# Performance work log

Hardware: AMD Instinct MI355X
Metric: run time of the kernel (lower is better)

Reference implementation:

```python
import jax, jax.numpy as jnp
import numpy as np

MARGIN = 2.0
N_STREAM = 4
BRANCH_WEIGHT = np.ones(N_STREAM, dtype=np.float32)  # default branch_weight = [1.0]*n_stream
ALPHA = 1.0 / N_STREAM  # MultistreamLoss default alpha
BETA = 1.0              # MultistreamLoss default beta
EPS = 1e-4


def _ranking(preds, labels):
    # sum over pairs i<j of relu(-(p[j]-p[i]) * sign(l[j]-l[i]) + margin)
    n = preds.shape[0]
    d = preds[None, :] - preds[:, None]          # d[i, j] = p[j] - p[i]
    s = jnp.sign(labels[None, :] - labels[:, None])
    h = jax.nn.relu(-d * s + MARGIN)             # [n, n]
    mask = jnp.triu(jnp.ones((n, n), dtype=bool), k=1)  # j > i
    return jnp.sum(jnp.where(mask, h, jnp.zeros((), h.dtype)))


def setup_inputs() -> dict:
    key = jax.random.key(0)
    k1, k2, k3 = jax.random.split(key, 3)
    n = 4096
    scores = jax.random.normal(k1, (N_STREAM, n), dtype=jnp.float32)
    pred = jax.random.normal(k2, (n,), dtype=jnp.float32)
    label = jax.random.normal(k3, (n,), dtype=jnp.float32)
    return {"scores": scores, "pred": pred, "label": label}


def reference(scores, pred, label):
    # branch ranking losses, one per stream
    branch = jax.vmap(lambda s: _ranking(s, label))(scores)       # [N_STREAM]
    branch_loss = jnp.sum(jnp.asarray(BRANCH_WEIGHT) * branch)

    # BatchRankingMSE_Loss (alpha=None -> 1.0, beta=None -> grad-norm ratio, no renorm)
    mse = jnp.mean((pred - label) ** 2)
    rank = _ranking(pred, label)
    g1 = jnp.linalg.norm(jax.grad(lambda p: jnp.mean((p - label) ** 2))(pred))
    g2 = jnp.linalg.norm(jax.grad(lambda p: _ranking(p, label))(pred))
    beta_w = jax.lax.stop_gradient(g1 / (g2 + EPS))  # computed under no_grad in torch
    pred_loss = 1.0 * mse + beta_w * rank

    return ALPHA * branch_loss + BETA * pred_loss
```

## Files before the change

### kernel.cpp

```cpp
#include <hip/hip_runtime.h>
#include <math.h>

#define N 4096
#define MARGINF 2.0f
#define EPSF 1e-4f

typedef _Float16 f16x2 __attribute__((ext_vector_type(2)));

__device__ __forceinline__ unsigned f2u(f16x2 h){ return __builtin_bit_cast(unsigned, h); }
__device__ __forceinline__ f16x2 u2f(unsigned u){ return __builtin_bit_cast(f16x2, u); }
__device__ __forceinline__ unsigned pku(float a, float b){
    return __builtin_bit_cast(unsigned, __builtin_amdgcn_cvt_pkrtz(a, b));
}
__device__ __forceinline__ f16x2 pk2(float a){ return u2f(pku(a, a)); }
__device__ __forceinline__ float fdot2(f16x2 a, f16x2 b, float c){
    return __builtin_amdgcn_fdot2(a, b, c, false);
}
__device__ __forceinline__ f16x2 c_one(){ return u2f(0x3C003C00u); }
__device__ __forceinline__ f16x2 c_two(){ return u2f(0x40004000u); }
__device__ __forceinline__ f16x2 c_zero(){ return u2f(0u); }
__device__ __forceinline__ f16x2 c_big(){ return u2f(0x7BFF7BFFu); }

constexpr int CC = 128;
constexpr int NCHUNK = N / CC;
constexpr int RTS = 1024;
constexpr int RTP = 512;
constexpr int SCORE_PER_STREAM = 80;
constexpr int NSCORE_BLK = 4 * SCORE_PER_STREAM;
constexpr int NPRED_BLK = (N / RTP) * NCHUNK;
constexpr int NBLK = NSCORE_BLK + NPRED_BLK;
constexpr int PRED_PART = 512;
constexpr int G16_BYTE_OFF = 4096;


__device__ __forceinline__ void body2(unsigned lm2u, unsigned pm2u,
                                      f16x2 lk2, f16x2 rk2, float& acc){
    const f16x2 ld2 = u2f(lm2u) - lk2;
    const unsigned sgn = f2u(ld2) & 0x80008000u;
    const f16x2 pd2 = u2f(pm2u) - rk2;
    const f16x2 x2 = u2f(f2u(pd2) ^ sgn);
    const f16x2 m2 = __builtin_elementwise_max(c_two() - x2, c_zero());
    acc = fdot2(m2, c_one(), acc);
}

__device__ __forceinline__ void body2m(unsigned lm2u, unsigned pm2u,
                                       f16x2 lk2, f16x2 rk2, int d, float& acc){
    const f16x2 ld2 = u2f(lm2u) - lk2;
    const unsigned sgn = f2u(ld2) & 0x80008000u;
    const f16x2 pd2 = u2f(pm2u) - rk2;
    const f16x2 x2 = u2f(f2u(pd2) ^ sgn);
    const f16x2 m2 = __builtin_elementwise_max(c_two() - x2, c_zero());
    const unsigned mu = (d >= 0) ? ((d > 0) ? 0x3C003C00u : 0x3C000000u) : 0u;
    acc = fdot2(m2, u2f(mu), acc);
}

__device__ __forceinline__ void body2g(unsigned lm2u, unsigned pm2u,
                                       f16x2 lk2, f16x2 rk2, float& acc, float& gacc){
    const f16x2 ld2 = u2f(lm2u) - lk2;
    const unsigned sgn = f2u(ld2) & 0x80008000u;
    const f16x2 pd2 = u2f(pm2u) - rk2;
    const f16x2 x2 = u2f(f2u(pd2) ^ sgn);
    const f16x2 m2 = __builtin_elementwise_max(c_two() - x2, c_zero());
    acc = fdot2(m2, c_one(), acc);
    const f16x2 ind2 = __builtin_elementwise_min(m2 * c_big(), c_one());
    gacc = fdot2(u2f(f2u(ind2) ^ sgn), c_one(), gacc);
}

__global__ __launch_bounds__(256) void pair_kernel(
    const float* __restrict__ scores, const float* __restrict__ pred,
    const float* __restrict__ label, float* __restrict__ ws)
{
    __shared__ unsigned lab16[CC / 2];
    __shared__ unsigned col16[CC / 2];
    __shared__ float red[4];

    const int bid = blockIdx.x;
    const int tid = threadIdx.x;
    const bool isScore = (bid < NSCORE_BLK);

    int ti, c, rb;
    const float* __restrict__ colsrc;
    if (isScore) {
        const int stream = bid / SCORE_PER_STREAM;
        const int b = bid % SCORE_PER_STREAM;
        if      (b < 32) { ti = 0; c = b; }
        else if (b < 56) { ti = 1; c = 8  + (b - 32); }
        else if (b < 72) { ti = 2; c = 16 + (b - 56); }
        else             { ti = 3; c = 24 + (b - 72); }
        rb = ti * RTS;
        colsrc = scores + stream * N;
    } else {
        const int q = bid - NSCORE_BLK;
        ti = q >> 5;
        c  = q & 31;
        rb = ti * RTP;
        colsrc = pred;
    }
    const int c0 = c * CC;

    if (tid < CC / 2) {
        const float2 lf = *(const float2*)&label[c0 + 2 * tid];
        lab16[tid] = pku(lf.x, lf.y);
    } else if (tid < CC) {
        const int q = tid - CC / 2;
        const float2 pf = *(const float2*)&colsrc[c0 + 2 * q];
        col16[q] = pku(pf.x, pf.y);
    }
    __syncthreads();

    float blocksum;

    if (isScore) {
        int r[4]; f16x2 rk2[4], lk2[4];
        #pragma unroll
        for (int k = 0; k < 4; ++k) {
            r[k] = rb + tid + 256 * k;
            rk2[k] = pk2(colsrc[r[k]]);
            lk2[k] = pk2(label[r[k]]);
        }
        float acc[8] = {0.f,0.f,0.f,0.f,0.f,0.f,0.f,0.f};

        if (c >= 8 * (ti + 1)) {
            #pragma unroll 4
            for (int q = 0; q < CC / 16; ++q) {
                const uint4 l4a = *(const uint4*)&lab16[q * 8];
                const uint4 s4a = *(const uint4*)&col16[q * 8];
                const uint4 l4b = *(const uint4*)&lab16[q * 8 + 4];
                const uint4 s4b = *(const uint4*)&col16[q * 8 + 4];
                #pragma unroll
                for (int k = 0; k < 4; ++k) {
                    body2(l4a.x, s4a.x, lk2[k], rk2[k], acc[k]);
                    body2(l4a.y, s4a.y, lk2[k], rk2[k], acc[4 + k]);
                    body2(l4a.z, s4a.z, lk2[k], rk2[k], acc[k]);
                    body2(l4a.w, s4a.w, lk2[k], rk2[k], acc[4 + k]);
                    body2(l4b.x, s4b.x, lk2[k], rk2[k], acc[k]);
                    body2(l4b.y, s4b.y, lk2[k], rk2[k], acc[4 + k]);
                    body2(l4b.z, s4b.z, lk2[k], rk2[k], acc[k]);
                    body2(l4b.w, s4b.w, lk2[k], rk2[k], acc[4 + k]);
                }
            }
        } else {
            #pragma unroll 4
            for (int q = 0; q < CC / 8; ++q) {
                const uint4 l4 = *(const uint4*)&lab16[q * 4];
                const uint4 s4 = *(const uint4*)&col16[q * 4];
                const int cb = c0 + q * 8;
                #pragma unroll
                for (int k = 0; k < 4; ++k) {
                    body2m(l4.x, s4.x, lk2[k], rk2[k], cb + 0 - r[k], acc[k]);
                    body2m(l4.y, s4.y, lk2[k], rk2[k], cb + 2 - r[k], acc[4 + k]);
                    body2m(l4.z, s4.z, lk2[k], rk2[k], cb + 4 - r[k], acc[k]);
                    body2m(l4.w, s4.w, lk2[k], rk2[k], cb + 6 - r[k], acc[4 + k]);
                }
            }
        }
        blocksum = (acc[0] + acc[1]) + (acc[2] + acc[3])
                 + (acc[4] + acc[5]) + (acc[6] + acc[7]);
    } else {
        int r[2]; f16x2 rk2[2], lk2[2];
        #pragma unroll
        for (int k = 0; k < 2; ++k) {
            r[k] = rb + tid + 256 * k;
            rk2[k] = pk2(pred[r[k]]);
            lk2[k] = pk2(label[r[k]]);
        }
        float acc[4] = {0.f,0.f,0.f,0.f};
        float grd[4] = {0.f,0.f,0.f,0.f};

        #pragma unroll 4
        for (int q = 0; q < CC / 8; ++q) {
            const uint4 l4 = *(const uint4*)&lab16[q * 4];
            const uint4 s4 = *(const uint4*)&col16[q * 4];
            #pragma unroll
            for (int k = 0; k < 2; ++k) {
                body2g(l4.x, s4.x, lk2[k], rk2[k], acc[k],     grd[k]);
                body2g(l4.y, s4.y, lk2[k], rk2[k], acc[2 + k], grd[2 + k]);
                body2g(l4.z, s4.z, lk2[k], rk2[k], acc[k],     grd[k]);
                body2g(l4.w, s4.w, lk2[k], rk2[k], acc[2 + k], grd[2 + k]);
            }
        }
        unsigned short* g16 = (unsigned short*)((char*)ws + G16_BYTE_OFF);
        #pragma unroll
        for (int k = 0; k < 2; ++k) {
            float g = grd[k] + grd[2 + k];
            if ((r[k] >> 7) == c) g -= 1.0f;
            const _Float16 gh = (_Float16)g;
            g16[r[k] * NCHUNK + c] = __builtin_bit_cast(unsigned short, gh);
        }
        blocksum = (acc[0] + acc[1]) + (acc[2] + acc[3]);
    }

    #pragma unroll
    for (int off = 32; off > 0; off >>= 1)
        blocksum += __shfl_xor(blocksum, off, 64);
    const int wid = tid >> 6;
    const int lane = tid & 63;
    if (lane == 0) red[wid] = blocksum;
    __syncthreads();
    if (tid == 0) {
        const float total = red[0] + red[1] + red[2] + red[3];
        if (isScore) ws[bid] = total;
        else         ws[PRED_PART + (bid - NSCORE_BLK)] = total;
    }
}

__global__ __launch_bounds__(256) void finalize_kernel(
    const float* __restrict__ pred, const float* __restrict__ label,
    const float* __restrict__ ws, float* __restrict__ out)
{
    __shared__ float lds[16];
    const int tid = threadIdx.x;
    const unsigned short* g16 = (const unsigned short*)((const char*)ws + G16_BYTE_OFF);

    float sse = 0.f, g2sq = 0.f;
    #pragma unroll
    for (int k = 0; k < 16; ++k) {
        const int i = k * 256 + tid;
        const float d = pred[i] - label[i];
        sse += d * d;
        const uint4* gp = (const uint4*)(g16 + i * NCHUNK);
        const uint4 a = gp[0], b = gp[1], cq = gp[2], e = gp[3];
        const f16x2 s0 = (u2f(a.x) + u2f(a.y)) + (u2f(a.z) + u2f(a.w));
        const f16x2 s1 = (u2f(b.x) + u2f(b.y)) + (u2f(b.z) + u2f(b.w));
        const f16x2 s2 = (u2f(cq.x) + u2f(cq.y)) + (u2f(cq.z) + u2f(cq.w));
        const f16x2 s3 = (u2f(e.x) + u2f(e.y)) + (u2f(e.z) + u2f(e.w));
        const f16x2 t0 = s0 + s1, t1 = s2 + s3;
        const float g = ((float)t0.x + (float)t0.y) + ((float)t1.x + (float)t1.y);
        g2sq += g * g;
    }

    float br = ws[tid] + ((tid < 64) ? ws[256 + tid] : 0.f);
    float pr = ws[PRED_PART + tid];

    #pragma unroll
    for (int off = 32; off > 0; off >>= 1) {
        sse  += __shfl_xor(sse,  off, 64);
        g2sq += __shfl_xor(g2sq, off, 64);
        br   += __shfl_xor(br,   off, 64);
        pr   += __shfl_xor(pr,   off, 64);
    }
    const int wid = tid >> 6;
    const int lane = tid & 63;
    if (lane == 0) {
        lds[wid] = sse; lds[4 + wid] = g2sq;
        lds[8 + wid] = br; lds[12 + wid] = pr;
    }
    __syncthreads();
    if (tid == 0) {
        const float sseT  = lds[0] + lds[1] + lds[2] + lds[3];
        const float g2sqT = lds[4] + lds[5] + lds[6] + lds[7];
        const float brT   = lds[8] + lds[9] + lds[10] + lds[11];
        const float prT   = lds[12] + lds[13] + lds[14] + lds[15];
        const float rankp = (prT - (float)N * MARGINF) * 0.5f;
        const float mse = sseT / (float)N;
        const float g1 = (2.0f / (float)N) * sqrtf(sseT);
        const float g2 = sqrtf(g2sqT);
        const float beta = g1 / (g2 + EPSF);
        out[0] = 0.25f * brT + mse + beta * rankp;
    }
}

extern "C" void kernel_launch(void* const* d_in, const int* in_sizes, int n_in,
                              void* d_out, int out_size, void* d_ws, size_t ws_size,
                              hipStream_t stream) {
    const float* scores = (const float*)d_in[0];
    const float* pred   = (const float*)d_in[1];
    const float* label  = (const float*)d_in[2];
    float* ws  = (float*)d_ws;
    float* out = (float*)d_out;

    pair_kernel<<<NBLK, 256, 0, stream>>>(scores, pred, label, ws);
    finalize_kernel<<<1, 256, 0, stream>>>(pred, label, ws, out);
}
```

Baseline: 24.73 us.

## Fuse pair and finalize kernels using per-block done tags and a spinning last block

```diff
diff --git a/kernel.cpp b/kernel.cpp
--- a/kernel.cpp
+++ b/kernel.cpp
@@ -30,7 +30,9 @@
 constexpr int NPRED_BLK = (N / RTP) * NCHUNK;
 constexpr int NBLK = NSCORE_BLK + NPRED_BLK;
 constexpr int PRED_PART = 512;
-constexpr int G16_BYTE_OFF = 4096;
+constexpr unsigned DONE_TAG = 0x3FA0B7C4u;
+constexpr int TAG_BYTE_OFF = 8192;
+constexpr int G16_BYTE_OFF = 16384;
 
 
 __device__ __forceinline__ void body2(unsigned lm2u, unsigned pm2u,
@@ -66,18 +68,11 @@
     gacc = fdot2(u2f(f2u(ind2) ^ sgn), c_one(), gacc);
 }
 
-__global__ __launch_bounds__(256) void pair_kernel(
+__device__ __forceinline__ float pair_phase(
     const float* __restrict__ scores, const float* __restrict__ pred,
-    const float* __restrict__ label, float* __restrict__ ws)
+    const float* __restrict__ label, float* __restrict__ ws,
+    unsigned* lab16, unsigned* col16, int bid, int tid, bool isScore)
 {
-    __shared__ unsigned lab16[CC / 2];
-    __shared__ unsigned col16[CC / 2];
-    __shared__ float red[4];
-
-    const int bid = blockIdx.x;
-    const int tid = threadIdx.x;
-    const bool isScore = (bid < NSCORE_BLK);
-
     int ti, c, rb;
     const float* __restrict__ colsrc;
     if (isScore) {
@@ -189,36 +184,22 @@
         }
         blocksum = (acc[0] + acc[1]) + (acc[2] + acc[3]);
     }
-
-    #pragma unroll
-    for (int off = 32; off > 0; off >>= 1)
-        blocksum += __shfl_xor(blocksum, off, 64);
-    const int wid = tid >> 6;
-    const int lane = tid & 63;
-    if (lane == 0) red[wid] = blocksum;
-    __syncthreads();
-    if (tid == 0) {
-        const float total = red[0] + red[1] + red[2] + red[3];
-        if (isScore) ws[bid] = total;
-        else         ws[PRED_PART + (bid - NSCORE_BLK)] = total;
-    }
-}
-
-__global__ __launch_bounds__(256) void finalize_kernel(
+    return blocksum;
+}
+
+__device__ __forceinline__ void finalize_phase(
     const float* __restrict__ pred, const float* __restrict__ label,
-    const float* __restrict__ ws, float* __restrict__ out)
+    const float* __restrict__ ws, float* __restrict__ out,
+    float* red, int tid)
 {
-    __shared__ float lds[16];
-    const int tid = threadIdx.x;
-    const unsigned short* g16 = (const unsigned short*)((const char*)ws + G16_BYTE_OFF);
-
+    const unsigned short* g16r = (const unsigned short*)((const char*)ws + G16_BYTE_OFF);
     float sse = 0.f, g2sq = 0.f;
     #pragma unroll
     for (int k = 0; k < 16; ++k) {
         const int i = k * 256 + tid;
         const float d = pred[i] - label[i];
         sse += d * d;
-        const uint4* gp = (const uint4*)(g16 + i * NCHUNK);
+        const uint4* gp = (const uint4*)(g16r + i * NCHUNK);
         const uint4 a = gp[0], b = gp[1], cq = gp[2], e = gp[3];
         const f16x2 s0 = (u2f(a.x) + u2f(a.y)) + (u2f(a.z) + u2f(a.w));
         const f16x2 s1 = (u2f(b.x) + u2f(b.y)) + (u2f(b.z) + u2f(b.w));
@@ -242,15 +223,15 @@
     const int wid = tid >> 6;
     const int lane = tid & 63;
     if (lane == 0) {
-        lds[wid] = sse; lds[4 + wid] = g2sq;
-        lds[8 + wid] = br; lds[12 + wid] = pr;
+        red[wid] = sse; red[4 + wid] = g2sq;
+        red[8 + wid] = br; red[12 + wid] = pr;
     }
     __syncthreads();
     if (tid == 0) {
-        const float sseT  = lds[0] + lds[1] + lds[2] + lds[3];
-        const float g2sqT = lds[4] + lds[5] + lds[6] + lds[7];
-        const float brT   = lds[8] + lds[9] + lds[10] + lds[11];
-        const float prT   = lds[12] + lds[13] + lds[14] + lds[15];
+        const float sseT  = red[0] + red[1] + red[2] + red[3];
+        const float g2sqT = red[4] + red[5] + red[6] + red[7];
+        const float brT   = red[8] + red[9] + red[10] + red[11];
+        const float prT   = red[12] + red[13] + red[14] + red[15];
         const float rankp = (prT - (float)N * MARGINF) * 0.5f;
         const float mse = sseT / (float)N;
         const float g1 = (2.0f / (float)N) * sqrtf(sseT);
@@ -258,6 +239,58 @@
         const float beta = g1 / (g2 + EPSF);
         out[0] = 0.25f * brT + mse + beta * rankp;
     }
+}
+
+__global__ __launch_bounds__(256) void fused_kernel(
+    const float* __restrict__ scores, const float* __restrict__ pred,
+    const float* __restrict__ label, float* __restrict__ ws,
+    float* __restrict__ out)
+{
+    __shared__ unsigned lab16[CC / 2];
+    __shared__ unsigned col16[CC / 2];
+    __shared__ float red[16];
+
+    const int bid = blockIdx.x;
+    const int tid = threadIdx.x;
+    unsigned* tags = (unsigned*)((char*)ws + TAG_BYTE_OFF);
+
+    if (bid < NBLK) {
+        const bool isScore = (bid < NSCORE_BLK);
+        float blocksum = pair_phase(scores, pred, label, ws, lab16, col16,
+                                    bid, tid, isScore);
+        #pragma unroll
+        for (int off = 32; off > 0; off >>= 1)
+            blocksum += __shfl_xor(blocksum, off, 64);
+        const int wid = tid >> 6;
+        const int lane = tid & 63;
+        if (lane == 0) red[wid] = blocksum;
+        __syncthreads();
+        if (tid == 0) {
+            const float total = red[0] + red[1] + red[2] + red[3];
+            if (isScore) ws[bid] = total;
+            else         ws[PRED_PART + (bid - NSCORE_BLK)] = total;
+        }
+        __threadfence();
+        __syncthreads();
+        if (tid == 0)
+            __hip_atomic_store(&tags[bid], DONE_TAG, __ATOMIC_RELEASE,
+                               __HIP_MEMORY_SCOPE_AGENT);
+        return;
+    }
+
+    for (int i = tid; i < NBLK; i += 256) {
+        while (__hip_atomic_load(&tags[i], __ATOMIC_ACQUIRE,
+                                 __HIP_MEMORY_SCOPE_AGENT) != DONE_TAG) {
+            __builtin_amdgcn_s_sleep(2);
+        }
+    }
+    __syncthreads();
+    __threadfence();
+    finalize_phase(pred, label, ws, out, red, tid);
+    __syncthreads();
+    for (int i = tid; i < NBLK; i += 256)
+        __hip_atomic_store(&tags[i], 0u, __ATOMIC_RELAXED,
+                           __HIP_MEMORY_SCOPE_AGENT);
 }
 
 extern "C" void kernel_launch(void* const* d_in, const int* in_sizes, int n_in,
@@ -269,6 +302,5 @@
     float* ws  = (float*)d_ws;
     float* out = (float*)d_out;
 
-    pair_kernel<<<NBLK, 256, 0, stream>>>(scores, pred, label, ws);
-    finalize_kernel<<<1, 256, 0, stream>>>(pred, label, ws, out);
-}
+    fused_kernel<<<NBLK + 1, 256, 0, stream>>>(scores, pred, label, ws, out);
+}
```

New measurement: 76.09 us. +207.7%, slower.

## Fuse pair and finalize kernels using an atomic counter and in-kernel finalizer block

Applied to the files above, without the earlier changes.

```diff
diff --git a/kernel.cpp b/kernel.cpp
--- a/kernel.cpp
+++ b/kernel.cpp
@@ -4,6 +4,7 @@
 #define N 4096
 #define MARGINF 2.0f
 #define EPSF 1e-4f
+#define SCOPE_AGENT __HIP_MEMORY_SCOPE_AGENT
 
 typedef _Float16 f16x2 __attribute__((ext_vector_type(2)));
 
@@ -22,16 +23,16 @@
 __device__ __forceinline__ f16x2 c_big(){ return u2f(0x7BFF7BFFu); }
 
 constexpr int CC = 128;
-constexpr int NCHUNK = N / CC;
+constexpr int SCORE_PER_STREAM = 80;
+constexpr int NPRED_BLK = 128;
+constexpr int NSCORE_BLK = 4 * SCORE_PER_STREAM;
+constexpr int NPROD = NPRED_BLK + NSCORE_BLK;
 constexpr int RTS = 1024;
-constexpr int RTP = 512;
-constexpr int SCORE_PER_STREAM = 80;
-constexpr int NSCORE_BLK = 4 * SCORE_PER_STREAM;
-constexpr int NPRED_BLK = (N / RTP) * NCHUNK;
-constexpr int NBLK = NSCORE_BLK + NPRED_BLK;
-constexpr int PRED_PART = 512;
-constexpr int G16_BYTE_OFF = 4096;
-
+
+constexpr int CTR_OFF = 0;
+constexpr int A_OFF   = 64;
+constexpr int B_OFF   = 640;
+constexpr int C_OFF   = 832;
 
 __device__ __forceinline__ void body2(unsigned lm2u, unsigned pm2u,
                                       f16x2 lk2, f16x2 rk2, float& acc){
@@ -66,77 +67,167 @@
     gacc = fdot2(u2f(f2u(ind2) ^ sgn), c_one(), gacc);
 }
 
-__global__ __launch_bounds__(256) void pair_kernel(
+__global__ __launch_bounds__(256) void fused_kernel(
     const float* __restrict__ scores, const float* __restrict__ pred,
-    const float* __restrict__ label, float* __restrict__ ws)
+    const float* __restrict__ label, float* __restrict__ ws,
+    float* __restrict__ out)
 {
-    __shared__ unsigned lab16[CC / 2];
-    __shared__ unsigned col16[CC / 2];
-    __shared__ float red[4];
-
+    __shared__ unsigned shm[2 * 2080];
+    __shared__ float red[16];
+
+    unsigned* wsu = (unsigned*)ws;
     const int bid = blockIdx.x;
     const int tid = threadIdx.x;
-    const bool isScore = (bid < NSCORE_BLK);
-
-    int ti, c, rb;
-    const float* __restrict__ colsrc;
-    if (isScore) {
-        const int stream = bid / SCORE_PER_STREAM;
-        const int b = bid % SCORE_PER_STREAM;
-        if      (b < 32) { ti = 0; c = b; }
-        else if (b < 56) { ti = 1; c = 8  + (b - 32); }
-        else if (b < 72) { ti = 2; c = 16 + (b - 56); }
-        else             { ti = 3; c = 24 + (b - 72); }
-        rb = ti * RTS;
-        colsrc = scores + stream * N;
+
+    if (bid == 0) {
+        if (tid == 0) {
+            const unsigned snap = __hip_atomic_load(wsu + CTR_OFF, __ATOMIC_RELAXED,
+                                                    SCOPE_AGENT);
+            unsigned guard = 0;
+            while ((__hip_atomic_load(wsu + CTR_OFF, __ATOMIC_RELAXED, SCOPE_AGENT)
+                    - snap) < (unsigned)NPROD) {
+                __builtin_amdgcn_s_sleep(8);
+                if (++guard > (1u << 27)) break;
+            }
+            __threadfence();
+        }
+        __syncthreads();
+
+        float br = 0.f, pr = 0.f, g2sq = 0.f, sse = 0.f;
+        {
+            const int b1 = 1 + tid;
+            const float a1 = __uint_as_float(__hip_atomic_load(
+                wsu + A_OFF + b1, __ATOMIC_RELAXED, SCOPE_AGENT));
+            if (b1 <= NPRED_BLK) pr += a1; else br += a1;
+            const int b2 = 257 + tid;
+            if (b2 <= NPROD) {
+                br += __uint_as_float(__hip_atomic_load(
+                    wsu + A_OFF + b2, __ATOMIC_RELAXED, SCOPE_AGENT));
+            }
+            if (tid < NPRED_BLK) {
+                g2sq = __uint_as_float(__hip_atomic_load(
+                    wsu + B_OFF + 1 + tid, __ATOMIC_RELAXED, SCOPE_AGENT));
+                sse  = __uint_as_float(__hip_atomic_load(
+                    wsu + C_OFF + 1 + tid, __ATOMIC_RELAXED, SCOPE_AGENT));
+            }
+        }
+        #pragma unroll
+        for (int off = 32; off > 0; off >>= 1) {
+            br   += __shfl_xor(br,   off, 64);
+            pr   += __shfl_xor(pr,   off, 64);
+            g2sq += __shfl_xor(g2sq, off, 64);
+            sse  += __shfl_xor(sse,  off, 64);
+        }
+        const int wid = tid >> 6;
+        const int lane = tid & 63;
+        if (lane == 0) {
+            red[wid] = br; red[4 + wid] = pr;
+            red[8 + wid] = g2sq; red[12 + wid] = sse;
+        }
+        __syncthreads();
+        if (tid == 0) {
+            const float brT   = red[0] + red[1] + red[2] + red[3];
+            const float prT   = red[4] + red[5] + red[6] + red[7];
+            const float g2sqT = red[8] + red[9] + red[10] + red[11];
+            const float sseT  = red[12] + red[13] + red[14] + red[15];
+            const float rankp = (prT - (float)N * MARGINF) * 0.5f;
+            const float mse = sseT / (float)N;
+            const float g1 = (2.0f / (float)N) * sqrtf(sseT);
+            const float g2 = sqrtf(g2sqT);
+            const float beta = g1 / (g2 + EPSF);
+            out[0] = 0.25f * brT + mse + beta * rankp;
+        }
+        return;
+    }
+
+    const bool isPred = (bid <= NPRED_BLK);
+    float rank_total, g2sq_total = 0.f, sse_total = 0.f;
+
+    if (isPred) {
+        const int rb = (bid - 1) * 32;
+        #pragma unroll
+        for (int q = 0; q < 8; ++q) {
+            const int j = q * 256 + tid;
+            const float2 lf = *(const float2*)&label[2 * j];
+            shm[q * 260 + tid] = pku(lf.x, lf.y);
+            const float2 pf = *(const float2*)&pred[2 * j];
+            shm[2080 + q * 260 + tid] = pku(pf.x, pf.y);
+        }
+        __syncthreads();
+
+        const int rowofs = tid >> 3;
+        const int cg = tid & 7;
+        const int r = rb + rowofs;
+        const f16x2 rk2 = pk2(pred[r]);
+        const f16x2 lk2 = pk2(label[r]);
+        const unsigned base = cg * 260;
+
+        float acc0 = 0.f, acc1 = 0.f, g0 = 0.f, g1v = 0.f;
+        #pragma unroll 4
+        for (int it = 0; it < 64; ++it) {
+            const uint4 l4 = *(const uint4*)&shm[base + it * 4];
+            const uint4 s4 = *(const uint4*)&shm[2080 + base + it * 4];
+            body2g(l4.x, s4.x, lk2, rk2, acc0, g0);
+            body2g(l4.y, s4.y, lk2, rk2, acc1, g1v);
+            body2g(l4.z, s4.z, lk2, rk2, acc0, g0);
+            body2g(l4.w, s4.w, lk2, rk2, acc1, g1v);
+        }
+        rank_total = acc0 + acc1;
+        float g = g0 + g1v;
+        if (cg == (r >> 9)) g -= 1.0f;
+        g += __shfl_xor(g, 1, 64);
+        g += __shfl_xor(g, 2, 64);
+        g += __shfl_xor(g, 4, 64);
+        if (cg == 0) {
+            g2sq_total = g * g;
+            const float d = pred[r] - label[r];
+            sse_total = d * d;
+        }
     } else {
-        const int q = bid - NSCORE_BLK;
-        ti = q >> 5;
-        c  = q & 31;
-        rb = ti * RTP;
-        colsrc = pred;
-    }
-    const int c0 = c * CC;
-
-    if (tid < CC / 2) {
-        const float2 lf = *(const float2*)&label[c0 + 2 * tid];
-        lab16[tid] = pku(lf.x, lf.y);
-    } else if (tid < CC) {
-        const int q = tid - CC / 2;
-        const float2 pf = *(const float2*)&colsrc[c0 + 2 * q];
-        col16[q] = pku(pf.x, pf.y);
-    }
-    __syncthreads();
-
-    float blocksum;
-
-    if (isScore) {
+        const int b = bid - 1 - NPRED_BLK;
+        const int stream = b / SCORE_PER_STREAM;
+        const int t = b % SCORE_PER_STREAM;
+        int ti, c;
+        if      (t < 32) { ti = 0; c = t; }
+        else if (t < 56) { ti = 1; c = 8  + (t - 32); }
+        else if (t < 72) { ti = 2; c = 16 + (t - 56); }
+        else             { ti = 3; c = 24 + (t - 72); }
+        const float* __restrict__ p = scores + stream * N;
+        const int c0 = c * CC;
+        unsigned* lab16 = shm;
+        unsigned* col16 = shm + 2080;
+
+        if (tid < CC / 2) {
+            const float2 lf = *(const float2*)&label[c0 + 2 * tid];
+            lab16[tid] = pku(lf.x, lf.y);
+        } else if (tid < CC) {
+            const int q = tid - CC / 2;
+            const float2 pf = *(const float2*)&p[c0 + 2 * q];
+            col16[q] = pku(pf.x, pf.y);
+        }
+        __syncthreads();
+
+        const int rb = ti * RTS;
         int r[4]; f16x2 rk2[4], lk2[4];
         #pragma unroll
         for (int k = 0; k < 4; ++k) {
             r[k] = rb + tid + 256 * k;
-            rk2[k] = pk2(colsrc[r[k]]);
+            rk2[k] = pk2(p[r[k]]);
             lk2[k] = pk2(label[r[k]]);
         }
         float acc[8] = {0.f,0.f,0.f,0.f,0.f,0.f,0.f,0.f};
 
         if (c >= 8 * (ti + 1)) {
             #pragma unroll 4
-            for (int q = 0; q < CC / 16; ++q) {
-                const uint4 l4a = *(const uint4*)&lab16[q * 8];
-                const uint4 s4a = *(const uint4*)&col16[q * 8];
-                const uint4 l4b = *(const uint4*)&lab16[q * 8 + 4];
-                const uint4 s4b = *(const uint4*)&col16[q * 8 + 4];
+            for (int q = 0; q < CC / 8; ++q) {
+                const uint4 l4 = *(const uint4*)&lab16[q * 4];
+                const uint4 s4 = *(const uint4*)&col16[q * 4];
                 #pragma unroll
                 for (int k = 0; k < 4; ++k) {
-                    body2(l4a.x, s4a.x, lk2[k], rk2[k], acc[k]);
-                    body2(l4a.y, s4a.y, lk2[k], rk2[k], acc[4 + k]);
-                    body2(l4a.z, s4a.z, lk2[k], rk2[k], acc[k]);
-                    body2(l4a.w, s4a.w, lk2[k], rk2[k], acc[4 + k]);
-                    body2(l4b.x, s4b.x, lk2[k], rk2[k], acc[k]);
-                    body2(l4b.y, s4b.y, lk2[k], rk2[k], acc[4 + k]);
-                    body2(l4b.z, s4b.z, lk2[k], rk2[k], acc[k]);
-                    body2(l4b.w, s4b.w, lk2[k], rk2[k], acc[4 + k]);
+                    body2(l4.x, s4.x, lk2[k], rk2[k], acc[k]);
+                    body2(l4.y, s4.y, lk2[k], rk2[k], acc[4 + k]);
+                    body2(l4.z, s4.z, lk2[k], rk2[k], acc[k]);
+                    body2(l4.w, s4.w, lk2[k], rk2[k], acc[4 + k]);
                 }
             }
         } else {
@@ -154,109 +245,35 @@
                 }
             }
         }
-        blocksum = (acc[0] + acc[1]) + (acc[2] + acc[3])
-                 + (acc[4] + acc[5]) + (acc[6] + acc[7]);
-    } else {
-        int r[2]; f16x2 rk2[2], lk2[2];
-        #pragma unroll
-        for (int k = 0; k < 2; ++k) {
-            r[k] = rb + tid + 256 * k;
-            rk2[k] = pk2(pred[r[k]]);
-            lk2[k] = pk2(label[r[k]]);
-        }
-        float acc[4] = {0.f,0.f,0.f,0.f};
-        float grd[4] = {0.f,0.f,0.f,0.f};
-
-        #pragma unroll 4
-        for (int q = 0; q < CC / 8; ++q) {
-            const uint4 l4 = *(const uint4*)&lab16[q * 4];
-            const uint4 s4 = *(const uint4*)&col16[q * 4];
-            #pragma unroll
-            for (int k = 0; k < 2; ++k) {
-                body2g(l4.x, s4.x, lk2[k], rk2[k], acc[k],     grd[k]);
-                body2g(l4.y, s4.y, lk2[k], rk2[k], acc[2 + k], grd[2 + k]);
-                body2g(l4.z, s4.z, lk2[k], rk2[k], acc[k],     grd[k]);
-                body2g(l4.w, s4.w, lk2[k], rk2[k], acc[2 + k], grd[2 + k]);
-            }
-        }
-        unsigned short* g16 = (unsigned short*)((char*)ws + G16_BYTE_OFF);
-        #pragma unroll
-        for (int k = 0; k < 2; ++k) {
-            float g = grd[k] + grd[2 + k];
-            if ((r[k] >> 7) == c) g -= 1.0f;
-            const _Float16 gh = (_Float16)g;
-            g16[r[k] * NCHUNK + c] = __builtin_bit_cast(unsigned short, gh);
-        }
-        blocksum = (acc[0] + acc[1]) + (acc[2] + acc[3]);
-    }
-
-    #pragma unroll
-    for (int off = 32; off > 0; off >>= 1)
-        blocksum += __shfl_xor(blocksum, off, 64);
-    const int wid = tid >> 6;
-    const int lane = tid & 63;
-    if (lane == 0) red[wid] = blocksum;
-    __syncthreads();
-    if (tid == 0) {
-        const float total = red[0] + red[1] + red[2] + red[3];
-        if (isScore) ws[bid] = total;
-        else         ws[PRED_PART + (bid - NSCORE_BLK)] = total;
-    }
-}
-
-__global__ __launch_bounds__(256) void finalize_kernel(
-    const float* __restrict__ pred, const float* __restrict__ label,
-    const float* __restrict__ ws, float* __restrict__ out)
-{
-    __shared__ float lds[16];
-    const int tid = threadIdx.x;
-    const unsigned short* g16 = (const unsigned short*)((const char*)ws + G16_BYTE_OFF);
-
-    float sse = 0.f, g2sq = 0.f;
-    #pragma unroll
-    for (int k = 0; k < 16; ++k) {
-        const int i = k * 256 + tid;
-        const float d = pred[i] - label[i];
-        sse += d * d;
-        const uint4* gp = (const uint4*)(g16 + i * NCHUNK);
-        const uint4 a = gp[0], b = gp[1], cq = gp[2], e = gp[3];
-        const f16x2 s0 = (u2f(a.x) + u2f(a.y)) + (u2f(a.z) + u2f(a.w));
-        const f16x2 s1 = (u2f(b.x) + u2f(b.y)) + (u2f(b.z) + u2f(b.w));
-        const f16x2 s2 = (u2f(cq.x) + u2f(cq.y)) + (u2f(cq.z) + u2f(cq.w));
-        const f16x2 s3 = (u2f(e.x) + u2f(e.y)) + (u2f(e.z) + u2f(e.w));
-        const f16x2 t0 = s0 + s1, t1 = s2 + s3;
-        const float g = ((float)t0.x + (float)t0.y) + ((float)t1.x + (float)t1.y);
-        g2sq += g * g;
-    }
-
-    float br = ws[tid] + ((tid < 64) ? ws[256 + tid] : 0.f);
-    float pr = ws[PRED_PART + tid];
+        rank_total = (acc[0] + acc[1]) + (acc[2] + acc[3])
+                   + (acc[4] + acc[5]) + (acc[6] + acc[7]);
+    }
 
     #pragma unroll
     for (int off = 32; off > 0; off >>= 1) {
-        sse  += __shfl_xor(sse,  off, 64);
-        g2sq += __shfl_xor(g2sq, off, 64);
-        br   += __shfl_xor(br,   off, 64);
-        pr   += __shfl_xor(pr,   off, 64);
+        rank_total += __shfl_xor(rank_total, off, 64);
+        g2sq_total += __shfl_xor(g2sq_total, off, 64);
+        sse_total  += __shfl_xor(sse_total,  off, 64);
     }
     const int wid = tid >> 6;
     const int lane = tid & 63;
     if (lane == 0) {
-        lds[wid] = sse; lds[4 + wid] = g2sq;
-        lds[8 + wid] = br; lds[12 + wid] = pr;
+        red[wid] = rank_total; red[4 + wid] = g2sq_total; red[8 + wid] = sse_total;
     }
     __syncthreads();
     if (tid == 0) {
-        const float sseT  = lds[0] + lds[1] + lds[2] + lds[3];
-        const float g2sqT = lds[4] + lds[5] + lds[6] + lds[7];
-        const float brT   = lds[8] + lds[9] + lds[10] + lds[11];
-        const float prT   = lds[12] + lds[13] + lds[14] + lds[15];
-        const float rankp = (prT - (float)N * MARGINF) * 0.5f;
-        const float mse = sseT / (float)N;
-        const float g1 = (2.0f / (float)N) * sqrtf(sseT);
-        const float g2 = sqrtf(g2sqT);
-        const float beta = g1 / (g2 + EPSF);
-        out[0] = 0.25f * brT + mse + beta * rankp;
+        const float rankT = red[0] + red[1] + red[2] + red[3];
+        __hip_atomic_store(wsu + A_OFF + bid, __float_as_uint(rankT),
+                           __ATOMIC_RELAXED, SCOPE_AGENT);
+        if (isPred) {
+            const float g2T  = red[4] + red[5] + red[6] + red[7];
+            const float sseT = red[8] + red[9] + red[10] + red[11];
+            __hip_atomic_store(wsu + B_OFF + bid, __float_as_uint(g2T),
+                               __ATOMIC_RELAXED, SCOPE_AGENT);
+            __hip_atomic_store(wsu + C_OFF + bid, __float_as_uint(sseT),
+                               __ATOMIC_RELAXED, SCOPE_AGENT);
+        }
+        __hip_atomic_fetch_add(wsu + CTR_OFF, 1u, __ATOMIC_RELEASE, SCOPE_AGENT);
     }
 }
 
@@ -269,6 +286,5 @@
     float* ws  = (float*)d_ws;
     float* out = (float*)d_out;
 
-    pair_kernel<<<NBLK, 256, 0, stream>>>(scores, pred, label, ws);
-    finalize_kernel<<<1, 256, 0, stream>>>(pred, label, ws, out);
-}
+    fused_kernel<<<NPROD + 1, 256, 0, stream>>>(scores, pred, label, ws, out);
+}
```

After: 20.10 us. -18.7%, faster.
